# Performance work log

Measured on AMD Instinct MI355X. Metric: run time of the kernel, lower is better.

The kernel has to match this reference:

```python
import jax, jax.numpy as jnp
import numpy as np

N_NODES = 100000
N_EDGES = 3200000
D_FEAT = 512
HIDDEN = 16
N_CLASSES = 16


def setup_inputs() -> dict:
    key = jax.random.key(0)
    ks = jax.random.split(key, 6)
    x = jax.random.normal(ks[0], (N_NODES, D_FEAT), dtype=jnp.float32)
    edge_index = jax.random.randint(ks[1], (2, N_EDGES), 0, N_NODES, dtype=jnp.int64)
    edge_weight = jax.random.uniform(ks[2], (N_EDGES,), dtype=jnp.float32)
    W1 = jax.random.normal(ks[3], (D_FEAT, HIDDEN), dtype=jnp.float32) * (1.0 / np.sqrt(D_FEAT))
    b1 = jnp.zeros((HIDDEN,), dtype=jnp.float32)
    W2 = jax.random.normal(ks[4], (HIDDEN, N_CLASSES), dtype=jnp.float32) * (1.0 / np.sqrt(HIDDEN))
    b2 = jnp.zeros((N_CLASSES,), dtype=jnp.float32)
    return {"x": x, "edge_index": edge_index, "edge_weight": edge_weight,
            "W1": W1, "b1": b1, "W2": W2, "b2": b2}


def _gcn_conv(h, src, dst, edge_weight, W, b, num_nodes):
    # linear transform then edge-weighted scatter-add: out[dst] += w_e * (h W)[src]
    h = h @ W                                   # [N, out]
    msg = edge_weight[:, None] * h[src]         # [E, out] gather + scale
    out = jax.ops.segment_sum(msg, dst, num_segments=num_nodes)  # scatter-add
    return out + b


def reference(x, edge_index, edge_weight, W1, b1, W2, b2):
    src, dst = edge_index[0], edge_index[1]
    n = x.shape[0]
    h = jax.nn.relu(_gcn_conv(x, src, dst, edge_weight, W1, b1, n))
    # dropout is identity in eval mode
    h = _gcn_conv(h, src, dst, edge_weight, W2, b2, n)
    return jax.nn.log_softmax(h, axis=1)
```

## Files before the change

### kernel.cpp

```cpp
#include <hip/hip_runtime.h>
#include <math.h>

#define NN 100000
#define DF 512
#define HID 16
#define NBUCK 392
#define EPB 4096

__device__ int g_idx64;

__global__ void detect_idx_kernel(const long long* __restrict__ idx) {
    int lane = threadIdx.x;
    int ok = 1;
    for (int i = lane; i < 128; i += 64) {
        long long v = idx[i];
        if (v < 0 || v >= NN) ok = 0;
    }
    unsigned long long m = __ballot(ok);
    if (lane == 0) g_idx64 = (m == ~0ULL);
}

__global__ __launch_bounds__(64) void gemm1_kernel(
    const float* __restrict__ x, const float* __restrict__ W1,
    float* __restrict__ h1, int nN)
{
    int node = blockIdx.x * 64 + threadIdx.x;
    if (node >= nN) return;
    const float4* xr = (const float4*)(x + (size_t)node * DF);

    float acc[16];
#pragma unroll
    for (int c = 0; c < 16; ++c) acc[c] = 0.f;

#pragma unroll 4
    for (int kq = 0; kq < DF / 4; ++kq) {
        float4 xv = xr[kq];
        const float* wrow = W1 + kq * 4 * HID;
        float xs[4] = {xv.x, xv.y, xv.z, xv.w};
#pragma unroll
        for (int j = 0; j < 4; ++j) {
            float s = xs[j];
#pragma unroll
            for (int c = 0; c < 16; ++c)
                acc[c] = fmaf(s, wrow[j * 16 + c], acc[c]);
        }
    }

    float4* o = (float4*)(h1 + (size_t)node * HID);
#pragma unroll
    for (int g = 0; g < 4; ++g)
        o[g] = make_float4(acc[g * 4 + 0], acc[g * 4 + 1],
                           acc[g * 4 + 2], acc[g * 4 + 3]);
}

__global__ __launch_bounds__(256) void bucket_hist_kernel(
    const void* __restrict__ eidx, int* __restrict__ bcnt, int nE)
{
    __shared__ int h[NBUCK];
    for (int i = threadIdx.x; i < NBUCK; i += 256) h[i] = 0;
    __syncthreads();
    const int i64 = g_idx64;
    int stride = gridDim.x * 256;
    for (int e = blockIdx.x * 256 + threadIdx.x; e < nE; e += stride) {
        int d;
        if (i64) d = (int)((const long long*)eidx)[nE + e];
        else     d = ((const int*)eidx)[nE + e];
        if ((unsigned)d < (unsigned)NN) atomicAdd(&h[d >> 8], 1);
    }
    __syncthreads();
    for (int i = threadIdx.x; i < NBUCK; i += 256)
        if (h[i]) atomicAdd(&bcnt[i], h[i]);
}

__global__ __launch_bounds__(512) void bucket_scan_kernel(
    const int* __restrict__ bcnt, int* __restrict__ bbase,
    int* __restrict__ cursor, int* __restrict__ rowStart)
{
    __shared__ int s[512];
    int t = threadIdx.x;
    int v = (t < NBUCK) ? bcnt[t] : 0;
    s[t] = v;
    __syncthreads();
    for (int off = 1; off < 512; off <<= 1) {
        int u = (t >= off) ? s[t - off] : 0;
        __syncthreads();
        s[t] += u;
        __syncthreads();
    }
    int excl = s[t] - v;
    if (t < NBUCK) { bbase[t] = excl; cursor[t] = excl; }
    if (t == NBUCK) bbase[t] = excl;
    if (t == NBUCK) rowStart[NN] = excl;
}

__global__ __launch_bounds__(256) void bucketA_kernel(
    const void* __restrict__ eidx, const float* __restrict__ ew,
    int* __restrict__ cursor, int2* __restrict__ packed, int nE)
{
    __shared__ int cnt[NBUCK];
    __shared__ int base[NBUCK];
    int t = threadIdx.x;
    for (int i = t; i < NBUCK; i += 256) cnt[i] = 0;
    __syncthreads();

    const int e0 = blockIdx.x * EPB;
    const int i64 = g_idx64;
    int lo[16]; float wv[16]; int bk[16];
#pragma unroll
    for (int i = 0; i < 16; ++i) {
        int e = e0 + t + i * 256;
        bk[i] = -1;
        if (e < nE) {
            int s, d;
            if (i64) {
                const long long* p = (const long long*)eidx;
                s = (int)p[e]; d = (int)p[nE + e];
            } else {
                const int* p = (const int*)eidx;
                s = p[e]; d = p[nE + e];
            }
            if ((unsigned)d < (unsigned)NN) {
                float w = ew[e];
                if ((unsigned)s >= (unsigned)NN) { s = 0; w = 0.f; }
                bk[i] = d >> 8;
                lo[i] = s | ((d & 255) << 20);
                wv[i] = w;
                atomicAdd(&cnt[bk[i]], 1);
            }
        }
    }
    __syncthreads();
    for (int i = t; i < NBUCK; i += 256)
        base[i] = (cnt[i] > 0) ? atomicAdd(&cursor[i], cnt[i]) : 0;
    __syncthreads();
    for (int i = t; i < NBUCK; i += 256) cnt[i] = 0;
    __syncthreads();
#pragma unroll
    for (int i = 0; i < 16; ++i) {
        if (bk[i] >= 0) {
            int r = atomicAdd(&cnt[bk[i]], 1);
            packed[base[bk[i]] + r] = make_int2(lo[i], __float_as_int(wv[i]));
        }
    }
}

__global__ __launch_bounds__(256) void bucketB_kernel(
    const int2* __restrict__ packed, const int* __restrict__ bbase,
    int* __restrict__ rowStart, int2* __restrict__ se, int nN)
{
    __shared__ int hcnt[256];
    __shared__ int wtot[4];
    int b = blockIdx.x;
    int t = threadIdx.x;
    int beg = bbase[b], end = bbase[b + 1];

    hcnt[t] = 0;
    __syncthreads();
    for (int p = beg + t; p < end; p += 256)
        atomicAdd(&hcnt[(packed[p].x >> 20) & 255], 1);
    __syncthreads();

    int v = hcnt[t];
    int incl = v;
#pragma unroll
    for (int off = 1; off < 64; off <<= 1) {
        int u = __shfl_up(incl, off, 64);
        if ((t & 63) >= off) incl += u;
    }
    if ((t & 63) == 63) wtot[t >> 6] = incl;
    __syncthreads();
    int woff = 0;
#pragma unroll
    for (int w = 0; w < 4; ++w) if (w < (t >> 6)) woff += wtot[w];
    int excl = incl - v + woff;

    int node = b * 256 + t;
    if (node < nN) rowStart[node] = beg + excl;
    __syncthreads();
    hcnt[t] = beg + excl;
    __syncthreads();

    for (int p = beg + t; p < end; p += 256) {
        int2 e = packed[p];
        int dl = (e.x >> 20) & 255;
        int pos = atomicAdd(&hcnt[dl], 1);
        se[pos] = make_int2(e.x & 0xFFFFF, e.y);
    }
}

__global__ __launch_bounds__(256) void gather_kernel(
    const int* __restrict__ rowStart, const int2* __restrict__ se,
    const float* __restrict__ h, float* __restrict__ agg, int nN)
{
    int t = blockIdx.x * 256 + threadIdx.x;
    int n = t >> 2;
    if (n >= nN) return;
    int c4 = t & 3;
    int beg = rowStart[n], end = rowStart[n + 1];
    const float4* h4 = (const float4*)h;
    float4 acc = make_float4(0.f, 0.f, 0.f, 0.f);
    for (int p = beg; p < end; ++p) {
        int2 e = se[p];
        float w = __int_as_float(e.y);
        float4 v = h4[(size_t)e.x * 4 + c4];
        acc.x = fmaf(w, v.x, acc.x);
        acc.y = fmaf(w, v.y, acc.y);
        acc.z = fmaf(w, v.z, acc.z);
        acc.w = fmaf(w, v.w, acc.w);
    }
    ((float4*)agg)[(size_t)n * 4 + c4] = acc;
}

__global__ __launch_bounds__(256) void transform_kernel(
    const float* __restrict__ agg1, const float* __restrict__ b1,
    const float* __restrict__ W2, float* __restrict__ h2, int nN)
{
    __shared__ float sW2[256];
    __shared__ float sb1[16];
    sW2[threadIdx.x] = W2[threadIdx.x];
    if (threadIdx.x < 16) sb1[threadIdx.x] = b1[threadIdx.x];
    __syncthreads();
    int n = blockIdx.x * 256 + threadIdx.x;
    if (n >= nN) return;
    const float4* r = (const float4*)(agg1 + (size_t)n * 16);
    float v[16];
#pragma unroll
    for (int g = 0; g < 4; ++g) {
        float4 a = r[g];
        v[g * 4 + 0] = fmaxf(a.x + sb1[g * 4 + 0], 0.f);
        v[g * 4 + 1] = fmaxf(a.y + sb1[g * 4 + 1], 0.f);
        v[g * 4 + 2] = fmaxf(a.z + sb1[g * 4 + 2], 0.f);
        v[g * 4 + 3] = fmaxf(a.w + sb1[g * 4 + 3], 0.f);
    }
    float acc[16];
#pragma unroll
    for (int c = 0; c < 16; ++c) acc[c] = 0.f;
#pragma unroll
    for (int k = 0; k < 16; ++k) {
        float s = v[k];
#pragma unroll
        for (int c = 0; c < 16; ++c)
            acc[c] = fmaf(s, sW2[k * 16 + c], acc[c]);
    }
    float4* o = (float4*)(h2 + (size_t)n * 16);
#pragma unroll
    for (int g = 0; g < 4; ++g)
        o[g] = make_float4(acc[g * 4 + 0], acc[g * 4 + 1], acc[g * 4 + 2], acc[g * 4 + 3]);
}

__global__ __launch_bounds__(256) void logsoftmax_kernel(
    const float* __restrict__ agg2, const float* __restrict__ b2,
    float* __restrict__ out, int nN)
{
    __shared__ float sb2[16];
    if (threadIdx.x < 16) sb2[threadIdx.x] = b2[threadIdx.x];
    __syncthreads();
    int n = blockIdx.x * 256 + threadIdx.x;
    if (n >= nN) return;
    const float4* r = (const float4*)(agg2 + (size_t)n * 16);
    float v[16];
#pragma unroll
    for (int g = 0; g < 4; ++g) {
        float4 a = r[g];
        v[g * 4 + 0] = a.x + sb2[g * 4 + 0];
        v[g * 4 + 1] = a.y + sb2[g * 4 + 1];
        v[g * 4 + 2] = a.z + sb2[g * 4 + 2];
        v[g * 4 + 3] = a.w + sb2[g * 4 + 3];
    }
    float m = v[0];
#pragma unroll
    for (int c = 1; c < 16; ++c) m = fmaxf(m, v[c]);
    float s = 0.f;
#pragma unroll
    for (int c = 0; c < 16; ++c) s += expf(v[c] - m);
    float l = m + logf(s);
    float4* o = (float4*)(out + (size_t)n * 16);
#pragma unroll
    for (int g = 0; g < 4; ++g)
        o[g] = make_float4(v[g * 4 + 0] - l, v[g * 4 + 1] - l,
                           v[g * 4 + 2] - l, v[g * 4 + 3] - l);
}

extern "C" void kernel_launch(void* const* d_in, const int* in_sizes, int n_in,
                              void* d_out, int out_size, void* d_ws, size_t ws_size,
                              hipStream_t stream)
{
    const float* x  = (const float*)d_in[0];
    const void*  ei = d_in[1];
    const float* ew = (const float*)d_in[2];
    const float* W1 = (const float*)d_in[3];
    const float* b1 = (const float*)d_in[4];
    const float* W2 = (const float*)d_in[5];
    const float* b2 = (const float*)d_in[6];
    float* out = (float*)d_out;

    const int N = NN;
    const int E = in_sizes[2];

    const size_t featB = (size_t)N * HID * sizeof(float);
    const size_t rowB  = (((size_t)(N + 1) * 4) + 255) & ~255ULL;
    const size_t bkB   = (((size_t)(NBUCK + 1) * 4) + 255) & ~255ULL;
    const size_t seB   = ((size_t)E * 8 + 255) & ~255ULL;

    char* w = (char*)d_ws;
    float* buf0 = (float*)w;      w += (featB + 255) & ~255ULL;
    float* buf1 = (float*)w;      w += (featB + 255) & ~255ULL;
    int*   rowStart = (int*)w;    w += rowB;
    int*   bcnt = (int*)w;        w += bkB;
    int*   bbase = (int*)w;       w += bkB;
    int*   cursor = (int*)w;      w += bkB;
    int2*  se = (int2*)w;         w += seB;
    int2*  packed = (int2*)w;     w += seB;

    detect_idx_kernel<<<1, 64, 0, stream>>>((const long long*)ei);
    gemm1_kernel<<<(N + 63) / 64, 64, 0, stream>>>(x, W1, buf0, N);

    const int nblocks4 = (N * 4 + 255) / 256;

    hipMemsetAsync(bcnt, 0, (size_t)NBUCK * 4, stream);
    bucket_hist_kernel<<<256, 256, 0, stream>>>(ei, bcnt, E);
    bucket_scan_kernel<<<1, 512, 0, stream>>>(bcnt, bbase, cursor, rowStart);
    bucketA_kernel<<<(E + EPB - 1) / EPB, 256, 0, stream>>>(ei, ew, cursor, packed, E);
    bucketB_kernel<<<NBUCK, 256, 0, stream>>>(packed, bbase, rowStart, se, N);

    gather_kernel<<<nblocks4, 256, 0, stream>>>(rowStart, se, buf0, buf1, N);
    transform_kernel<<<(N + 255) / 256, 256, 0, stream>>>(buf1, b1, W2, buf0, N);
    gather_kernel<<<nblocks4, 256, 0, stream>>>(rowStart, se, buf0, buf1, N);
    logsoftmax_kernel<<<(N + 255) / 256, 256, 0, stream>>>(buf1, b2, out, N);
}
```

Before: 570.6 us.

## Fuse epilogues into gather, split-K gemm1, vectorize hist, stage buckets in LDS

The bias+ReLU+W2 transform and the bias+log_softmax are folded into the two gather kernels using wave shuffles, removing two kernel launches and their intermediate round trips through global memory. The gathers are also unrolled by four to keep more loads in flight. gemm1 now splits the K dimension across two waves per node and reduces the halves through shared memory to raise parallelism. The histogram reads destination indices two at a time, and bucketB stages its bucket in LDS so packed is read from global only once. The large LDS stage array may reduce occupancy in bucketB.

```diff
diff --git a/kernel.cpp b/kernel.cpp
--- a/kernel.cpp
+++ b/kernel.cpp
@@ -6,6 +6,7 @@
 #define HID 16
 #define NBUCK 392
 #define EPB 4096
+#define BCAP 7800
 
 __device__ int g_idx64;
 
@@ -20,37 +21,53 @@
     if (lane == 0) g_idx64 = (m == ~0ULL);
 }
 
-__global__ __launch_bounds__(64) void gemm1_kernel(
+__global__ __launch_bounds__(256) void gemm1_kernel(
     const float* __restrict__ x, const float* __restrict__ W1,
     float* __restrict__ h1, int nN)
 {
-    int node = blockIdx.x * 64 + threadIdx.x;
-    if (node >= nN) return;
-    const float4* xr = (const float4*)(x + (size_t)node * DF);
+    __shared__ float part[2][16 * 64];
+    int w    = threadIdx.x >> 6;
+    int lane = threadIdx.x & 63;
+    int pair = w >> 1;
+    int half = w & 1;
+    int node = blockIdx.x * 128 + pair * 64 + lane;
+    bool alive = node < nN;
 
     float acc[16];
 #pragma unroll
     for (int c = 0; c < 16; ++c) acc[c] = 0.f;
 
+    if (alive) {
+        const float4* xr = (const float4*)(x + (size_t)node * DF) + half * (DF / 8);
+        const float* wb = W1 + half * (DF / 2) * HID;
 #pragma unroll 4
-    for (int kq = 0; kq < DF / 4; ++kq) {
-        float4 xv = xr[kq];
-        const float* wrow = W1 + kq * 4 * HID;
-        float xs[4] = {xv.x, xv.y, xv.z, xv.w};
-#pragma unroll
-        for (int j = 0; j < 4; ++j) {
-            float s = xs[j];
-#pragma unroll
-            for (int c = 0; c < 16; ++c)
-                acc[c] = fmaf(s, wrow[j * 16 + c], acc[c]);
-        }
-    }
-
-    float4* o = (float4*)(h1 + (size_t)node * HID);
-#pragma unroll
-    for (int g = 0; g < 4; ++g)
-        o[g] = make_float4(acc[g * 4 + 0], acc[g * 4 + 1],
-                           acc[g * 4 + 2], acc[g * 4 + 3]);
+        for (int kq = 0; kq < DF / 8; ++kq) {
+            float4 xv = xr[kq];
+            const float* wrow = wb + kq * 4 * HID;
+            float xs[4] = {xv.x, xv.y, xv.z, xv.w};
+#pragma unroll
+            for (int j = 0; j < 4; ++j) {
+                float s = xs[j];
+#pragma unroll
+                for (int c = 0; c < 16; ++c)
+                    acc[c] = fmaf(s, wrow[j * 16 + c], acc[c]);
+            }
+        }
+    }
+    if (half == 1) {
+#pragma unroll
+        for (int c = 0; c < 16; ++c) part[pair][c * 64 + lane] = acc[c];
+    }
+    __syncthreads();
+    if (half == 0 && alive) {
+#pragma unroll
+        for (int c = 0; c < 16; ++c) acc[c] += part[pair][c * 64 + lane];
+        float4* o = (float4*)(h1 + (size_t)node * HID);
+#pragma unroll
+        for (int g = 0; g < 4; ++g)
+            o[g] = make_float4(acc[g * 4 + 0], acc[g * 4 + 1],
+                               acc[g * 4 + 2], acc[g * 4 + 3]);
+    }
 }
 
 __global__ __launch_bounds__(256) void bucket_hist_kernel(
@@ -61,11 +78,31 @@
     __syncthreads();
     const int i64 = g_idx64;
     int stride = gridDim.x * 256;
-    for (int e = blockIdx.x * 256 + threadIdx.x; e < nE; e += stride) {
-        int d;
-        if (i64) d = (int)((const long long*)eidx)[nE + e];
-        else     d = ((const int*)eidx)[nE + e];
-        if ((unsigned)d < (unsigned)NN) atomicAdd(&h[d >> 8], 1);
+    int tid = blockIdx.x * 256 + threadIdx.x;
+    if ((nE & 1) == 0) {
+        int nE2 = nE >> 1;
+        if (i64) {
+            const int4* dp = (const int4*)((const long long*)eidx + nE);
+            for (int i = tid; i < nE2; i += stride) {
+                int4 d = dp[i];
+                if (d.y == 0 && (unsigned)d.x < (unsigned)NN) atomicAdd(&h[d.x >> 8], 1);
+                if (d.w == 0 && (unsigned)d.z < (unsigned)NN) atomicAdd(&h[d.z >> 8], 1);
+            }
+        } else {
+            const int2* dp = (const int2*)((const int*)eidx + nE);
+            for (int i = tid; i < nE2; i += stride) {
+                int2 d = dp[i];
+                if ((unsigned)d.x < (unsigned)NN) atomicAdd(&h[d.x >> 8], 1);
+                if ((unsigned)d.y < (unsigned)NN) atomicAdd(&h[d.y >> 8], 1);
+            }
+        }
+    } else {
+        for (int e = tid; e < nE; e += stride) {
+            int d;
+            if (i64) d = (int)((const long long*)eidx)[nE + e];
+            else     d = ((const int*)eidx)[nE + e];
+            if ((unsigned)d < (unsigned)NN) atomicAdd(&h[d >> 8], 1);
+        }
     }
     __syncthreads();
     for (int i = threadIdx.x; i < NBUCK; i += 256)
@@ -150,14 +187,19 @@
 {
     __shared__ int hcnt[256];
     __shared__ int wtot[4];
+    __shared__ int2 stage[BCAP];
     int b = blockIdx.x;
     int t = threadIdx.x;
     int beg = bbase[b], end = bbase[b + 1];
+    int cnt = end - beg;
 
     hcnt[t] = 0;
     __syncthreads();
-    for (int p = beg + t; p < end; p += 256)
-        atomicAdd(&hcnt[(packed[p].x >> 20) & 255], 1);
+    for (int i = t; i < cnt; i += 256) {
+        int2 e = packed[beg + i];
+        if (i < BCAP) stage[i] = e;
+        atomicAdd(&hcnt[(e.x >> 20) & 255], 1);
+    }
     __syncthreads();
 
     int v = hcnt[t];
@@ -180,105 +222,101 @@
     hcnt[t] = beg + excl;
     __syncthreads();
 
-    for (int p = beg + t; p < end; p += 256) {
-        int2 e = packed[p];
+    for (int i = t; i < cnt; i += 256) {
+        int2 e = (i < BCAP) ? stage[i] : packed[beg + i];
         int dl = (e.x >> 20) & 255;
         int pos = atomicAdd(&hcnt[dl], 1);
         se[pos] = make_int2(e.x & 0xFFFFF, e.y);
     }
 }
 
-__global__ __launch_bounds__(256) void gather_kernel(
+template <int EPI>
+__global__ __launch_bounds__(256) void gather_fused_kernel(
     const int* __restrict__ rowStart, const int2* __restrict__ se,
-    const float* __restrict__ h, float* __restrict__ agg, int nN)
-{
+    const float* __restrict__ h, const float* __restrict__ bias,
+    const float* __restrict__ Wn, float* __restrict__ outp, int nN)
+{
+    __shared__ float sW[256];
+    __shared__ float sb[16];
+    if (EPI == 0) sW[threadIdx.x] = Wn[threadIdx.x];
+    if (threadIdx.x < 16) sb[threadIdx.x] = bias[threadIdx.x];
+    __syncthreads();
+
     int t = blockIdx.x * 256 + threadIdx.x;
     int n = t >> 2;
     if (n >= nN) return;
     int c4 = t & 3;
     int beg = rowStart[n], end = rowStart[n + 1];
     const float4* h4 = (const float4*)h;
-    float4 acc = make_float4(0.f, 0.f, 0.f, 0.f);
-    for (int p = beg; p < end; ++p) {
+
+    float ax = 0.f, ay = 0.f, az = 0.f, aw = 0.f;
+    int p = beg;
+    for (; p + 4 <= end; p += 4) {
+        int2 e0 = se[p], e1 = se[p + 1], e2 = se[p + 2], e3 = se[p + 3];
+        float4 v0 = h4[(size_t)(unsigned)e0.x * 4 + c4];
+        float4 v1 = h4[(size_t)(unsigned)e1.x * 4 + c4];
+        float4 v2 = h4[(size_t)(unsigned)e2.x * 4 + c4];
+        float4 v3 = h4[(size_t)(unsigned)e3.x * 4 + c4];
+        float w0 = __int_as_float(e0.y), w1 = __int_as_float(e1.y);
+        float w2 = __int_as_float(e2.y), w3 = __int_as_float(e3.y);
+        ax = fmaf(w0, v0.x, ax); ay = fmaf(w0, v0.y, ay);
+        az = fmaf(w0, v0.z, az); aw = fmaf(w0, v0.w, aw);
+        ax = fmaf(w1, v1.x, ax); ay = fmaf(w1, v1.y, ay);
+        az = fmaf(w1, v1.z, az); aw = fmaf(w1, v1.w, aw);
+        ax = fmaf(w2, v2.x, ax); ay = fmaf(w2, v2.y, ay);
+        az = fmaf(w2, v2.z, az); aw = fmaf(w2, v2.w, aw);
+        ax = fmaf(w3, v3.x, ax); ay = fmaf(w3, v3.y, ay);
+        az = fmaf(w3, v3.z, az); aw = fmaf(w3, v3.w, aw);
+    }
+    for (; p < end; ++p) {
         int2 e = se[p];
+        float4 v = h4[(size_t)(unsigned)e.x * 4 + c4];
         float w = __int_as_float(e.y);
-        float4 v = h4[(size_t)e.x * 4 + c4];
-        acc.x = fmaf(w, v.x, acc.x);
-        acc.y = fmaf(w, v.y, acc.y);
-        acc.z = fmaf(w, v.z, acc.z);
-        acc.w = fmaf(w, v.w, acc.w);
-    }
-    ((float4*)agg)[(size_t)n * 4 + c4] = acc;
-}
-
-__global__ __launch_bounds__(256) void transform_kernel(
-    const float* __restrict__ agg1, const float* __restrict__ b1,
-    const float* __restrict__ W2, float* __restrict__ h2, int nN)
-{
-    __shared__ float sW2[256];
-    __shared__ float sb1[16];
-    sW2[threadIdx.x] = W2[threadIdx.x];
-    if (threadIdx.x < 16) sb1[threadIdx.x] = b1[threadIdx.x];
-    __syncthreads();
-    int n = blockIdx.x * 256 + threadIdx.x;
-    if (n >= nN) return;
-    const float4* r = (const float4*)(agg1 + (size_t)n * 16);
-    float v[16];
-#pragma unroll
-    for (int g = 0; g < 4; ++g) {
-        float4 a = r[g];
-        v[g * 4 + 0] = fmaxf(a.x + sb1[g * 4 + 0], 0.f);
-        v[g * 4 + 1] = fmaxf(a.y + sb1[g * 4 + 1], 0.f);
-        v[g * 4 + 2] = fmaxf(a.z + sb1[g * 4 + 2], 0.f);
-        v[g * 4 + 3] = fmaxf(a.w + sb1[g * 4 + 3], 0.f);
-    }
-    float acc[16];
-#pragma unroll
-    for (int c = 0; c < 16; ++c) acc[c] = 0.f;
-#pragma unroll
-    for (int k = 0; k < 16; ++k) {
-        float s = v[k];
-#pragma unroll
-        for (int c = 0; c < 16; ++c)
-            acc[c] = fmaf(s, sW2[k * 16 + c], acc[c]);
-    }
-    float4* o = (float4*)(h2 + (size_t)n * 16);
-#pragma unroll
-    for (int g = 0; g < 4; ++g)
-        o[g] = make_float4(acc[g * 4 + 0], acc[g * 4 + 1], acc[g * 4 + 2], acc[g * 4 + 3]);
-}
-
-__global__ __launch_bounds__(256) void logsoftmax_kernel(
-    const float* __restrict__ agg2, const float* __restrict__ b2,
-    float* __restrict__ out, int nN)
-{
-    __shared__ float sb2[16];
-    if (threadIdx.x < 16) sb2[threadIdx.x] = b2[threadIdx.x];
-    __syncthreads();
-    int n = blockIdx.x * 256 + threadIdx.x;
-    if (n >= nN) return;
-    const float4* r = (const float4*)(agg2 + (size_t)n * 16);
-    float v[16];
-#pragma unroll
-    for (int g = 0; g < 4; ++g) {
-        float4 a = r[g];
-        v[g * 4 + 0] = a.x + sb2[g * 4 + 0];
-        v[g * 4 + 1] = a.y + sb2[g * 4 + 1];
-        v[g * 4 + 2] = a.z + sb2[g * 4 + 2];
-        v[g * 4 + 3] = a.w + sb2[g * 4 + 3];
-    }
-    float m = v[0];
-#pragma unroll
-    for (int c = 1; c < 16; ++c) m = fmaxf(m, v[c]);
-    float s = 0.f;
-#pragma unroll
-    for (int c = 0; c < 16; ++c) s += expf(v[c] - m);
-    float l = m + logf(s);
-    float4* o = (float4*)(out + (size_t)n * 16);
-#pragma unroll
-    for (int g = 0; g < 4; ++g)
-        o[g] = make_float4(v[g * 4 + 0] - l, v[g * 4 + 1] - l,
-                           v[g * 4 + 2] - l, v[g * 4 + 3] - l);
+        ax = fmaf(w, v.x, ax); ay = fmaf(w, v.y, ay);
+        az = fmaf(w, v.z, az); aw = fmaf(w, v.w, aw);
+    }
+
+    int lane = threadIdx.x & 63;
+    int lb = lane & ~3;
+
+    if (EPI == 0) {
+        float v0 = fmaxf(ax + sb[c4 * 4 + 0], 0.f);
+        float v1 = fmaxf(ay + sb[c4 * 4 + 1], 0.f);
+        float v2 = fmaxf(az + sb[c4 * 4 + 2], 0.f);
+        float v3 = fmaxf(aw + sb[c4 * 4 + 3], 0.f);
+        float vk[16];
+#pragma unroll
+        for (int j = 0; j < 4; ++j) {
+            vk[4 * j + 0] = __shfl(v0, lb + j, 64);
+            vk[4 * j + 1] = __shfl(v1, lb + j, 64);
+            vk[4 * j + 2] = __shfl(v2, lb + j, 64);
+            vk[4 * j + 3] = __shfl(v3, lb + j, 64);
+        }
+        float o0 = 0.f, o1 = 0.f, o2 = 0.f, o3 = 0.f;
+#pragma unroll
+        for (int k = 0; k < 16; ++k) {
+            float s = vk[k];
+            o0 = fmaf(s, sW[k * 16 + c4 * 4 + 0], o0);
+            o1 = fmaf(s, sW[k * 16 + c4 * 4 + 1], o1);
+            o2 = fmaf(s, sW[k * 16 + c4 * 4 + 2], o2);
+            o3 = fmaf(s, sW[k * 16 + c4 * 4 + 3], o3);
+        }
+        ((float4*)outp)[(size_t)n * 4 + c4] = make_float4(o0, o1, o2, o3);
+    } else {
+        float v0 = ax + sb[c4 * 4 + 0];
+        float v1 = ay + sb[c4 * 4 + 1];
+        float v2 = az + sb[c4 * 4 + 2];
+        float v3 = aw + sb[c4 * 4 + 3];
+        float m = fmaxf(fmaxf(v0, v1), fmaxf(v2, v3));
+        m = fmaxf(m, __shfl_xor(m, 1, 64));
+        m = fmaxf(m, __shfl_xor(m, 2, 64));
+        float s = expf(v0 - m) + expf(v1 - m) + expf(v2 - m) + expf(v3 - m);
+        s += __shfl_xor(s, 1, 64);
+        s += __shfl_xor(s, 2, 64);
+        float l = m + logf(s);
+        ((float4*)outp)[(size_t)n * 4 + c4] =
+            make_float4(v0 - l, v1 - l, v2 - l, v3 - l);
+    }
 }
 
 extern "C" void kernel_launch(void* const* d_in, const int* in_sizes, int n_in,
@@ -313,7 +351,7 @@
     int2*  packed = (int2*)w;     w += seB;
 
     detect_idx_kernel<<<1, 64, 0, stream>>>((const long long*)ei);
-    gemm1_kernel<<<(N + 63) / 64, 64, 0, stream>>>(x, W1, buf0, N);
+    gemm1_kernel<<<(N + 127) / 128, 256, 0, stream>>>(x, W1, buf0, N);
 
     const int nblocks4 = (N * 4 + 255) / 256;
 
@@ -323,8 +361,6 @@
     bucketA_kernel<<<(E + EPB - 1) / EPB, 256, 0, stream>>>(ei, ew, cursor, packed, E);
     bucketB_kernel<<<NBUCK, 256, 0, stream>>>(packed, bbase, rowStart, se, N);
 
-    gather_kernel<<<nblocks4, 256, 0, stream>>>(rowStart, se, buf0, buf1, N);
-    transform_kernel<<<(N + 255) / 256, 256, 0, stream>>>(buf1, b1, W2, buf0, N);
-    gather_kernel<<<nblocks4, 256, 0, stream>>>(rowStart, se, buf0, buf1, N);
-    logsoftmax_kernel<<<(N + 255) / 256, 256, 0, stream>>>(buf1, b2, out, N);
-}
+    gather_fused_kernel<0><<<nblocks4, 256, 0, stream>>>(rowStart, se, buf0, b1, W2, buf1, N);
+    gather_fused_kernel<1><<<nblocks4, 256, 0, stream>>>(rowStart, se, buf1, b2, W2, out, N);
+}
```

New measurement: 603.8 us. 5.8% more time.
